# Kernel tuning notes

Measured on AMD Instinct MI355X. Metric: run time of the kernel, lower is better.

## Reference

```python
import jax, jax.numpy as jnp
import numpy as np

V = 1_000_000   # sparse_id_num
D = 64          # embedding_dim
F = 26          # sparse_feature_cnt
L = 8           # ids per feature bag (fixed-size ragged regularization)
B = 4096        # batch
IN_DIM = F * D  # 1664
HIDDENS = (1024, 1024, 512)


def setup_inputs() -> dict:
    key = jax.random.key(0)
    ks = jax.random.split(key, 4 + 4 * len(HIDDENS))
    inp = {}
    inp["x"] = jax.random.randint(ks[0], (B, F, L), 0, V, dtype=jnp.int64)
    inp["emb_table"] = jax.random.normal(ks[1], (V, D), dtype=jnp.float32) * 0.01
    ki = 2
    for i, h in enumerate(HIDDENS):
        inp[f"w1_{i}"] = jax.random.normal(ks[ki], (IN_DIM, h), dtype=jnp.float32) * 0.02
        inp[f"b1_{i}"] = jnp.zeros((h,), dtype=jnp.float32)
        inp[f"w2_{i}"] = jax.random.normal(ks[ki + 1], (h, IN_DIM), dtype=jnp.float32) * 0.02
        inp[f"b2_{i}"] = jnp.zeros((IN_DIM,), dtype=jnp.float32)
        ki += 2
    inp["lin_w"] = jax.random.normal(ks[ki], (IN_DIM, 1), dtype=jnp.float32) * 0.02
    inp["lin_b"] = jnp.zeros((1,), dtype=jnp.float32)
    return inp


def reference(x, emb_table,
              w1_0, b1_0, w2_0, b2_0,
              w1_1, b1_1, w2_1, b2_1,
              w1_2, b1_2, w2_2, b2_2,
              lin_w, lin_b):
    # Batched embedding lookup + sum-pool over bag dim + concat over features.
    # x: [B, F, L] -> gather [B, F, L, D] -> sum over L -> [B, F, D] -> [B, F*D]
    pooled = emb_table[x].sum(axis=2)              # [B, F, D]
    feat = pooled.reshape(x.shape[0], -1)          # [B, F*D]
    # Residual blocks: relu(linear2(relu(linear1(x))) + x)
    for w1, b1, w2, b2 in ((w1_0, b1_0, w2_0, b2_0),
                           (w1_1, b1_1, w2_1, b2_1),
                           (w1_2, b1_2, w2_2, b2_2)):
        h = jax.nn.relu(feat @ w1 + b1)
        feat = jax.nn.relu(h @ w2 + b2 + feat)
    return jax.nn.sigmoid(feat @ lin_w + lin_b)    # [B, 1]
```

## Files before the change

kernel.cpp:

```cpp
#include <hip/hip_runtime.h>
#include <hip/hip_bf16.h>

#define BATCH 4096
#define FEATS 26
#define BAG   8
#define EDIM  64
#define INDIM 1664

typedef short bf16x8 __attribute__((ext_vector_type(8)));
typedef float f32x4  __attribute__((ext_vector_type(4)));
typedef unsigned short u16x8 __attribute__((ext_vector_type(8)));

__device__ __forceinline__ unsigned short f2bf(float f) {
    unsigned u = __float_as_uint(f);
    unsigned r = (u + 0x7FFFu + ((u >> 16) & 1u)) >> 16;
    return (unsigned short)r;
}
__device__ __forceinline__ float bf2f(unsigned short h) {
    return __uint_as_float((unsigned)h << 16);
}
__device__ __forceinline__ void async_cp16(const void* g, void* lds_base_uniform) {
    __builtin_amdgcn_global_load_lds(
        (const __attribute__((address_space(1))) unsigned int*)g,
        (__attribute__((address_space(3))) unsigned int*)lds_base_uniform,
        16, 0, 0);
}
#define WAITCNT_VM(n) __builtin_amdgcn_s_waitcnt(0x0F70 | (n))

__global__ __launch_bounds__(256) void transpose_to_bf16(
    const float* __restrict__ in, unsigned short* __restrict__ out, int R, int C)
{
    __shared__ unsigned short tile[64][65];
    const int c0 = blockIdx.x * 64, r0 = blockIdx.y * 64;
    const int t = threadIdx.x;
    const int tc = t & 63, tr = t >> 6;
#pragma unroll
    for (int i = 0; i < 16; ++i) {
        int r = tr + i * 4;
        tile[r][tc] = f2bf(in[(long long)(r0 + r) * C + c0 + tc]);
    }
    __syncthreads();
    const int wr = t >> 3, wc = t & 7;
#pragma unroll
    for (int half = 0; half < 2; ++half) {
        int row = wr + half * 32;
        u16x8 v;
#pragma unroll
        for (int j = 0; j < 8; ++j) v[j] = tile[wc * 8 + j][row];
        *(u16x8*)(out + (long long)(c0 + row) * R + r0 + wc * 8) = v;
    }
}

__global__ __launch_bounds__(256) void embed_pool(
    const int* __restrict__ x, const float* __restrict__ emb,
    unsigned short* __restrict__ feat)
{
    int bag  = blockIdx.x * 4 + (threadIdx.x >> 6);
    int lane = threadIdx.x & 63;
    int b = bag / FEATS;
    int f = bag - b * FEATS;
    const int* xs = x + (long long)bag * BAG;
    float s = 0.f;
#pragma unroll
    for (int l = 0; l < BAG; ++l) {
        int id = xs[l];
        s += emb[(long long)id * EDIM + lane];
    }
    feat[(long long)b * INDIM + f * EDIM + lane] = f2bf(s);
}

#define NBUF 4
__global__ __launch_bounds__(512) void gemm_bf16(
    const unsigned short* __restrict__ A, const unsigned short* __restrict__ Wt,
    const float* __restrict__ bias, const unsigned short* __restrict__ res,
    unsigned short* __restrict__ out, int M, int N, int K, int do_relu)
{
    __shared__ unsigned short As[NBUF * 128 * 32];
    __shared__ unsigned short Bs[NBUF * 128 * 32];

    const int t    = threadIdx.x;
    const int bCol = blockIdx.x * 128;
    const int bRow = blockIdx.y * 128;
    const int wave = t >> 6, lane = t & 63;
    const int wm = wave & 1, wn = wave >> 1;
    const int lm = lane & 15, quad = lane >> 4;

    const int srow = lane >> 2;
    const int sq   = (lane & 3) ^ ((lane >> 3) & 3);
    const unsigned short* Ag = A  + (long long)(bRow + wave * 16 + srow) * K + sq * 8;
    const unsigned short* Bg = Wt + (long long)(bCol + wave * 16 + srow) * K + sq * 8;
    unsigned short* AsW = As + wave * 512;
    unsigned short* BsW = Bs + wave * 512;

    const int T = K / 32;
    f32x4 acc[4][2] = {};

    const int slot = (quad ^ ((lm >> 1) & 3)) * 8;

#define ISSUE(tile_)  do { int _b = (tile_) & (NBUF - 1);                         \
        async_cp16(Ag + (long long)(tile_) * 32, AsW + _b * 4096);                \
        async_cp16(Bg + (long long)(tile_) * 32, BsW + _b * 4096); } while (0)

#define COMPUTE(tile_) do { int _b = (tile_) & (NBUF - 1);                        \
        const unsigned short* _a = As + _b * 4096;                                \
        const unsigned short* _bp = Bs + _b * 4096;                               \
        bf16x8 af[4], bf[2];                                                      \
        _Pragma("unroll")                                                         \
        for (int i = 0; i < 4; ++i)                                               \
            af[i] = *(const bf16x8*)&_a[(wm * 64 + i * 16 + lm) * 32 + slot];     \
        _Pragma("unroll")                                                         \
        for (int j = 0; j < 2; ++j)                                               \
            bf[j] = *(const bf16x8*)&_bp[(wn * 32 + j * 16 + lm) * 32 + slot];    \
        _Pragma("unroll")                                                         \
        for (int i = 0; i < 4; ++i)                                               \
            _Pragma("unroll")                                                     \
            for (int j = 0; j < 2; ++j)                                           \
                acc[i][j] = __builtin_amdgcn_mfma_f32_16x16x32_bf16(              \
                    af[i], bf[j], acc[i][j], 0, 0, 0); } while (0)

    ISSUE(0);
    ISSUE(1);
    for (int tt = 0; tt < T - 2; ++tt) {
        ISSUE(tt + 2);
        WAITCNT_VM(4);
        asm volatile("" ::: "memory");
        __builtin_amdgcn_s_barrier();
        asm volatile("" ::: "memory");
        COMPUTE(tt);
    }
    WAITCNT_VM(2);
    asm volatile("" ::: "memory");
    __builtin_amdgcn_s_barrier();
    asm volatile("" ::: "memory");
    COMPUTE(T - 2);
    WAITCNT_VM(0);
    asm volatile("" ::: "memory");
    __builtin_amdgcn_s_barrier();
    asm volatile("" ::: "memory");
    COMPUTE(T - 1);

#pragma unroll
    for (int i = 0; i < 4; ++i) {
#pragma unroll
        for (int j = 0; j < 2; ++j) {
            int col = bCol + wn * 32 + j * 16 + lm;
            float bv = bias[col];
#pragma unroll
            for (int r = 0; r < 4; ++r) {
                int row = bRow + wm * 64 + i * 16 + quad * 4 + r;
                float v = acc[i][j][r] + bv;
                if (res) v += bf2f(res[(long long)row * N + col]);
                if (do_relu) v = fmaxf(v, 0.f);
                out[(long long)row * N + col] = f2bf(v);
            }
        }
    }
#undef ISSUE
#undef COMPUTE
}

__global__ __launch_bounds__(256) void final_head(
    const unsigned short* __restrict__ feat, const float* __restrict__ lin_w,
    const float* __restrict__ lin_b, float* __restrict__ out)
{
    int row  = blockIdx.x * 4 + (threadIdx.x >> 6);
    int lane = threadIdx.x & 63;
    const unsigned short* fr = feat + (long long)row * INDIM;
    float s = 0.f;
#pragma unroll
    for (int it = 0; it < INDIM / 64; ++it)
        s += bf2f(fr[it * 64 + lane]) * lin_w[it * 64 + lane];
#pragma unroll
    for (int off = 32; off; off >>= 1)
        s += __shfl_down(s, off, 64);
    if (lane == 0)
        out[row] = 1.f / (1.f + __expf(-(s + lin_b[0])));
}

extern "C" void kernel_launch(void* const* d_in, const int* in_sizes, int n_in,
                              void* d_out, int out_size, void* d_ws, size_t ws_size,
                              hipStream_t stream) {
    const int*   x    = (const int*)  d_in[0];
    const float* emb  = (const float*)d_in[1];
    const float* w1_0 = (const float*)d_in[2];
    const float* b1_0 = (const float*)d_in[3];
    const float* w2_0 = (const float*)d_in[4];
    const float* b2_0 = (const float*)d_in[5];
    const float* w1_1 = (const float*)d_in[6];
    const float* b1_1 = (const float*)d_in[7];
    const float* w2_1 = (const float*)d_in[8];
    const float* b2_1 = (const float*)d_in[9];
    const float* w1_2 = (const float*)d_in[10];
    const float* b1_2 = (const float*)d_in[11];
    const float* w2_2 = (const float*)d_in[12];
    const float* b2_2 = (const float*)d_in[13];
    const float* linw = (const float*)d_in[14];
    const float* linb = (const float*)d_in[15];
    float* out = (float*)d_out;

    unsigned short* feat = (unsigned short*)d_ws;
    unsigned short* h    = feat + (long long)BATCH * INDIM;
    unsigned short* p    = h + (long long)BATCH * 1024;
    unsigned short* w1_0t = p; p += 1024 * INDIM;
    unsigned short* w2_0t = p; p += INDIM * 1024;
    unsigned short* w1_1t = p; p += 1024 * INDIM;
    unsigned short* w2_1t = p; p += INDIM * 1024;
    unsigned short* w1_2t = p; p += 512 * INDIM;
    unsigned short* w2_2t = p; p += INDIM * 512;

    transpose_to_bf16<<<dim3(1024/64, INDIM/64), 256, 0, stream>>>(w1_0, w1_0t, INDIM, 1024);
    transpose_to_bf16<<<dim3(INDIM/64, 1024/64), 256, 0, stream>>>(w2_0, w2_0t, 1024, INDIM);
    transpose_to_bf16<<<dim3(1024/64, INDIM/64), 256, 0, stream>>>(w1_1, w1_1t, INDIM, 1024);
    transpose_to_bf16<<<dim3(INDIM/64, 1024/64), 256, 0, stream>>>(w2_1, w2_1t, 1024, INDIM);
    transpose_to_bf16<<<dim3(512/64,  INDIM/64), 256, 0, stream>>>(w1_2, w1_2t, INDIM, 512);
    transpose_to_bf16<<<dim3(INDIM/64, 512/64),  256, 0, stream>>>(w2_2, w2_2t, 512, INDIM);

    embed_pool<<<BATCH * FEATS / 4, 256, 0, stream>>>(x, emb, feat);

    gemm_bf16<<<dim3(1024/128, BATCH/128), 512, 0, stream>>>(
        feat, w1_0t, b1_0, nullptr, h, BATCH, 1024, INDIM, 1);
    gemm_bf16<<<dim3(INDIM/128, BATCH/128), 512, 0, stream>>>(
        h, w2_0t, b2_0, feat, feat, BATCH, INDIM, 1024, 1);
    gemm_bf16<<<dim3(1024/128, BATCH/128), 512, 0, stream>>>(
        feat, w1_1t, b1_1, nullptr, h, BATCH, 1024, INDIM, 1);
    gemm_bf16<<<dim3(INDIM/128, BATCH/128), 512, 0, stream>>>(
        h, w2_1t, b2_1, feat, feat, BATCH, INDIM, 1024, 1);
    gemm_bf16<<<dim3(512/128, BATCH/128), 512, 0, stream>>>(
        feat, w1_2t, b1_2, nullptr, h, BATCH, 512, INDIM, 1);
    gemm_bf16<<<dim3(INDIM/128, BATCH/128), 512, 0, stream>>>(
        h, w2_2t, b2_2, feat, feat, BATCH, INDIM, 512, 1);

    final_head<<<BATCH / 4, 256, 0, stream>>>(feat, linw, linb, out);
}
```

Measured before the change: 568.6 us.

## Merge weight transposes into one launch and window embedding gathers by address

The six weight-transpose launches become one 3D-grid kernel that picks its matrix from blockIdx.z, with out-of-range blocks exiting early. The embedding pooling now has each wave handle four bags and loads all 32 ids up front. It then walks 31 address windows of 2M floats each, issuing only the gathers whose row falls in the current window. This is meant to keep concurrent gathers across the GPU in a narrow part of the 256MB table for better cache and TLB locality, and to save launch overhead. The cost is 31 passes of predicate checks per wave, and the loop stays correct only because every offset lies below 31·2^21.

After: 763.0 us. +34.2%, slower.

```diff
diff --git a/kernel.cpp b/kernel.cpp
--- a/kernel.cpp
+++ b/kernel.cpp
@@ -1,5 +1,4 @@
 #include <hip/hip_runtime.h>
-#include <hip/hip_bf16.h>
 
 #define BATCH 4096
 #define FEATS 26
@@ -27,11 +26,27 @@
 }
 #define WAITCNT_VM(n) __builtin_amdgcn_s_waitcnt(0x0F70 | (n))
 
-__global__ __launch_bounds__(256) void transpose_to_bf16(
-    const float* __restrict__ in, unsigned short* __restrict__ out, int R, int C)
-{
+__global__ __launch_bounds__(256) void transpose_all(
+    const float* __restrict__ w10, unsigned short* __restrict__ o10,
+    const float* __restrict__ w20, unsigned short* __restrict__ o20,
+    const float* __restrict__ w11, unsigned short* __restrict__ o11,
+    const float* __restrict__ w21, unsigned short* __restrict__ o21,
+    const float* __restrict__ w12, unsigned short* __restrict__ o12,
+    const float* __restrict__ w22, unsigned short* __restrict__ o22)
+{
+    const float* in; unsigned short* out; int R, C;
+    switch (blockIdx.z) {
+        case 0:  in = w10; out = o10; R = INDIM; C = 1024;  break;
+        case 1:  in = w20; out = o20; R = 1024;  C = INDIM; break;
+        case 2:  in = w11; out = o11; R = INDIM; C = 1024;  break;
+        case 3:  in = w21; out = o21; R = 1024;  C = INDIM; break;
+        case 4:  in = w12; out = o12; R = INDIM; C = 512;   break;
+        default: in = w22; out = o22; R = 512;   C = INDIM; break;
+    }
+    const int c0 = blockIdx.x * 64, r0 = blockIdx.y * 64;
+    if (c0 >= C || r0 >= R) return;
+
     __shared__ unsigned short tile[64][65];
-    const int c0 = blockIdx.x * 64, r0 = blockIdx.y * 64;
     const int t = threadIdx.x;
     const int tc = t & 63, tr = t >> 6;
 #pragma unroll
@@ -51,22 +66,39 @@
     }
 }
 
+#define BPW 4
+#define NWIN 31
 __global__ __launch_bounds__(256) void embed_pool(
     const int* __restrict__ x, const float* __restrict__ emb,
     unsigned short* __restrict__ feat)
 {
-    int bag  = blockIdx.x * 4 + (threadIdx.x >> 6);
-    int lane = threadIdx.x & 63;
-    int b = bag / FEATS;
-    int f = bag - b * FEATS;
-    const int* xs = x + (long long)bag * BAG;
-    float s = 0.f;
-#pragma unroll
-    for (int l = 0; l < BAG; ++l) {
-        int id = xs[l];
-        s += emb[(long long)id * EDIM + lane];
-    }
-    feat[(long long)b * INDIM + f * EDIM + lane] = f2bf(s);
+    const int wave = threadIdx.x >> 6, lane = threadIdx.x & 63;
+    const int bag0 = (blockIdx.x * 4 + wave) * BPW;
+    const float* embl = emb + lane;
+
+    unsigned off[BPW][BAG];
+#pragma unroll
+    for (int g = 0; g < BPW; ++g)
+#pragma unroll
+        for (int l = 0; l < BAG; ++l)
+            off[g][l] = (unsigned)x[(bag0 + g) * BAG + l] * (unsigned)EDIM;
+
+    float s[BPW] = {};
+#pragma unroll 1
+    for (unsigned w = 0; w < NWIN; ++w) {
+#pragma unroll
+        for (int g = 0; g < BPW; ++g)
+#pragma unroll
+            for (int l = 0; l < BAG; ++l)
+                if ((off[g][l] >> 21) == w)
+                    s[g] += embl[off[g][l]];
+    }
+#pragma unroll
+    for (int g = 0; g < BPW; ++g) {
+        int bag = bag0 + g;
+        int b = bag / FEATS, f = bag - b * FEATS;
+        feat[(long long)b * INDIM + f * EDIM + lane] = f2bf(s[g]);
+    }
 }
 
 #define NBUF 4
@@ -94,7 +126,6 @@
 
     const int T = K / 32;
     f32x4 acc[4][2] = {};
-
     const int slot = (quad ^ ((lm >> 1) & 3)) * 8;
 
 #define ISSUE(tile_)  do { int _b = (tile_) & (NBUF - 1);                         \
@@ -208,14 +239,10 @@
     unsigned short* w1_2t = p; p += 512 * INDIM;
     unsigned short* w2_2t = p; p += INDIM * 512;
 
-    transpose_to_bf16<<<dim3(1024/64, INDIM/64), 256, 0, stream>>>(w1_0, w1_0t, INDIM, 1024);
-    transpose_to_bf16<<<dim3(INDIM/64, 1024/64), 256, 0, stream>>>(w2_0, w2_0t, 1024, INDIM);
-    transpose_to_bf16<<<dim3(1024/64, INDIM/64), 256, 0, stream>>>(w1_1, w1_1t, INDIM, 1024);
-    transpose_to_bf16<<<dim3(INDIM/64, 1024/64), 256, 0, stream>>>(w2_1, w2_1t, 1024, INDIM);
-    transpose_to_bf16<<<dim3(512/64,  INDIM/64), 256, 0, stream>>>(w1_2, w1_2t, INDIM, 512);
-    transpose_to_bf16<<<dim3(INDIM/64, 512/64),  256, 0, stream>>>(w2_2, w2_2t, 512, INDIM);
-
-    embed_pool<<<BATCH * FEATS / 4, 256, 0, stream>>>(x, emb, feat);
+    transpose_all<<<dim3(26, 26, 6), 256, 0, stream>>>(
+        w1_0, w1_0t, w2_0, w2_0t, w1_1, w1_1t, w2_1, w2_1t, w1_2, w1_2t, w2_2, w2_2t);
+
+    embed_pool<<<BATCH * FEATS / (4 * BPW), 256, 0, stream>>>(x, emb, feat);
 
     gemm_bf16<<<dim3(1024/128, BATCH/128), 512, 0, stream>>>(
         feat, w1_0t, b1_0, nullptr, h, BATCH, 1024, INDIM, 1);
```

## Use 4-wave GEMM blocks with double buffering and batch weight transposes

Applied to the files above, without the earlier changes.

The GEMM moves from 8 waves per block with a 4-deep async LDS pipeline to 4 waves per block with launch bounds allowing 3 blocks per CU and a 2-stage buffer. Each wave now computes a 64x64 (or 64x32) sub-tile, and the kernel is templated on BN so the N=512 layer uses 64-wide tiles to get more blocks. The six weight-transpose launches are merged into one 3D-grid launch to cut launch overhead. The shallower pipeline and the full waitcnt plus barrier on every K step may expose more memory latency, relying on extra occupancy to hide it.

New measurement: 603.0 us. 6.1% more time.

```diff
diff --git a/kernel.cpp b/kernel.cpp
--- a/kernel.cpp
+++ b/kernel.cpp
@@ -1,5 +1,4 @@
 #include <hip/hip_runtime.h>
-#include <hip/hip_bf16.h>
 
 #define BATCH 4096
 #define FEATS 26
@@ -27,11 +26,27 @@
 }
 #define WAITCNT_VM(n) __builtin_amdgcn_s_waitcnt(0x0F70 | (n))
 
-__global__ __launch_bounds__(256) void transpose_to_bf16(
-    const float* __restrict__ in, unsigned short* __restrict__ out, int R, int C)
-{
+__global__ __launch_bounds__(256) void transpose_all(
+    const float* __restrict__ w10, unsigned short* __restrict__ o10,
+    const float* __restrict__ w20, unsigned short* __restrict__ o20,
+    const float* __restrict__ w11, unsigned short* __restrict__ o11,
+    const float* __restrict__ w21, unsigned short* __restrict__ o21,
+    const float* __restrict__ w12, unsigned short* __restrict__ o12,
+    const float* __restrict__ w22, unsigned short* __restrict__ o22)
+{
+    const float* in; unsigned short* out; int R, C;
+    switch (blockIdx.z) {
+        case 0:  in = w10; out = o10; R = INDIM; C = 1024;  break;
+        case 1:  in = w20; out = o20; R = 1024;  C = INDIM; break;
+        case 2:  in = w11; out = o11; R = INDIM; C = 1024;  break;
+        case 3:  in = w21; out = o21; R = 1024;  C = INDIM; break;
+        case 4:  in = w12; out = o12; R = INDIM; C = 512;   break;
+        default: in = w22; out = o22; R = 512;   C = INDIM; break;
+    }
+    const int c0 = blockIdx.x * 64, r0 = blockIdx.y * 64;
+    if (c0 >= C || r0 >= R) return;
+
     __shared__ unsigned short tile[64][65];
-    const int c0 = blockIdx.x * 64, r0 = blockIdx.y * 64;
     const int t = threadIdx.x;
     const int tc = t & 63, tr = t >> 6;
 #pragma unroll
@@ -69,17 +84,20 @@
     feat[(long long)b * INDIM + f * EDIM + lane] = f2bf(s);
 }
 
-#define NBUF 4
-__global__ __launch_bounds__(512) void gemm_bf16(
+#define NBUF 2
+template<int BN>
+__global__ __launch_bounds__(256, 3) void gemm_bf16(
     const unsigned short* __restrict__ A, const unsigned short* __restrict__ Wt,
     const float* __restrict__ bias, const unsigned short* __restrict__ res,
     unsigned short* __restrict__ out, int M, int N, int K, int do_relu)
 {
+    constexpr int JN = BN / 32;
+
     __shared__ unsigned short As[NBUF * 128 * 32];
-    __shared__ unsigned short Bs[NBUF * 128 * 32];
+    __shared__ unsigned short Bs[NBUF * BN * 32];
 
     const int t    = threadIdx.x;
-    const int bCol = blockIdx.x * 128;
+    const int bCol = blockIdx.x * BN;
     const int bRow = blockIdx.y * 128;
     const int wave = t >> 6, lane = t & 63;
     const int wm = wave & 1, wn = wave >> 1;
@@ -87,63 +105,62 @@
 
     const int srow = lane >> 2;
     const int sq   = (lane & 3) ^ ((lane >> 3) & 3);
-    const unsigned short* Ag = A  + (long long)(bRow + wave * 16 + srow) * K + sq * 8;
-    const unsigned short* Bg = Wt + (long long)(bCol + wave * 16 + srow) * K + sq * 8;
-    unsigned short* AsW = As + wave * 512;
-    unsigned short* BsW = Bs + wave * 512;
+    const int slot = (quad ^ ((lm >> 1) & 3)) * 8;
+
+    const unsigned short* Ag  = A + (long long)(bRow + wave * 32 + srow) * K + sq * 8;
+    const unsigned short* Ag2 = Ag + 16 * (long long)K;
+    const unsigned short* Bg  = Wt + (long long)(bCol + (BN == 128 ? wave * 32 : wave * 16) + srow) * K + sq * 8;
+    const unsigned short* Bg2 = Bg + 16 * (long long)K;
+    unsigned short* AsW = As + wave * 1024;
+    unsigned short* BsW = Bs + wave * (BN == 128 ? 1024 : 512);
 
     const int T = K / 32;
-    f32x4 acc[4][2] = {};
-
-    const int slot = (quad ^ ((lm >> 1) & 3)) * 8;
-
-#define ISSUE(tile_)  do { int _b = (tile_) & (NBUF - 1);                         \
-        async_cp16(Ag + (long long)(tile_) * 32, AsW + _b * 4096);                \
-        async_cp16(Bg + (long long)(tile_) * 32, BsW + _b * 4096); } while (0)
-
-#define COMPUTE(tile_) do { int _b = (tile_) & (NBUF - 1);                        \
-        const unsigned short* _a = As + _b * 4096;                                \
-        const unsigned short* _bp = Bs + _b * 4096;                               \
-        bf16x8 af[4], bf[2];                                                      \
+    f32x4 acc[4][JN] = {};
+
+#define ISSUE(t_)  do { int _b = (t_) & 1;                                        \
+        async_cp16(Ag  + (t_) * 32, AsW + _b * 4096);                             \
+        async_cp16(Ag2 + (t_) * 32, AsW + _b * 4096 + 512);                       \
+        async_cp16(Bg  + (t_) * 32, BsW + _b * (BN * 32));                        \
+        if constexpr (BN == 128)                                                  \
+            async_cp16(Bg2 + (t_) * 32, BsW + _b * (BN * 32) + 512);              \
+    } while (0)
+
+#define COMPUTE(t_) do { int _b = (t_) & 1;                                       \
+        const unsigned short* _a  = As + _b * 4096;                               \
+        const unsigned short* _bp = Bs + _b * (BN * 32);                          \
+        bf16x8 af[4], bfr[JN];                                                    \
         _Pragma("unroll")                                                         \
         for (int i = 0; i < 4; ++i)                                               \
             af[i] = *(const bf16x8*)&_a[(wm * 64 + i * 16 + lm) * 32 + slot];     \
         _Pragma("unroll")                                                         \
-        for (int j = 0; j < 2; ++j)                                               \
-            bf[j] = *(const bf16x8*)&_bp[(wn * 32 + j * 16 + lm) * 32 + slot];    \
+        for (int j = 0; j < JN; ++j)                                              \
+            bfr[j] = *(const bf16x8*)&_bp[(wn * (BN / 2) + j * 16 + lm) * 32 + slot]; \
         _Pragma("unroll")                                                         \
         for (int i = 0; i < 4; ++i)                                               \
             _Pragma("unroll")                                                     \
-            for (int j = 0; j < 2; ++j)                                           \
+            for (int j = 0; j < JN; ++j)                                          \
                 acc[i][j] = __builtin_amdgcn_mfma_f32_16x16x32_bf16(              \
-                    af[i], bf[j], acc[i][j], 0, 0, 0); } while (0)
+                    af[i], bfr[j], acc[i][j], 0, 0, 0); } while (0)
 
     ISSUE(0);
-    ISSUE(1);
-    for (int tt = 0; tt < T - 2; ++tt) {
-        ISSUE(tt + 2);
-        WAITCNT_VM(4);
-        asm volatile("" ::: "memory");
-        __builtin_amdgcn_s_barrier();
-        asm volatile("" ::: "memory");
-        COMPUTE(tt);
-    }
-    WAITCNT_VM(2);
-    asm volatile("" ::: "memory");
-    __builtin_amdgcn_s_barrier();
-    asm volatile("" ::: "memory");
-    COMPUTE(T - 2);
     WAITCNT_VM(0);
     asm volatile("" ::: "memory");
     __builtin_amdgcn_s_barrier();
     asm volatile("" ::: "memory");
-    COMPUTE(T - 1);
+    for (int tt = 0; tt < T; ++tt) {
+        if (tt + 1 < T) ISSUE(tt + 1);
+        COMPUTE(tt);
+        WAITCNT_VM(0);
+        asm volatile("" ::: "memory");
+        __builtin_amdgcn_s_barrier();
+        asm volatile("" ::: "memory");
+    }
 
 #pragma unroll
     for (int i = 0; i < 4; ++i) {
 #pragma unroll
-        for (int j = 0; j < 2; ++j) {
-            int col = bCol + wn * 32 + j * 16 + lm;
+        for (int j = 0; j < JN; ++j) {
+            int col = bCol + wn * (BN / 2) + j * 16 + lm;
             float bv = bias[col];
 #pragma unroll
             for (int r = 0; r < 4; ++r) {
@@ -208,26 +225,22 @@
     unsigned short* w1_2t = p; p += 512 * INDIM;
     unsigned short* w2_2t = p; p += INDIM * 512;
 
-    transpose_to_bf16<<<dim3(1024/64, INDIM/64), 256, 0, stream>>>(w1_0, w1_0t, INDIM, 1024);
-    transpose_to_bf16<<<dim3(INDIM/64, 1024/64), 256, 0, stream>>>(w2_0, w2_0t, 1024, INDIM);
-    transpose_to_bf16<<<dim3(1024/64, INDIM/64), 256, 0, stream>>>(w1_1, w1_1t, INDIM, 1024);
-    transpose_to_bf16<<<dim3(INDIM/64, 1024/64), 256, 0, stream>>>(w2_1, w2_1t, 1024, INDIM);
-    transpose_to_bf16<<<dim3(512/64,  INDIM/64), 256, 0, stream>>>(w1_2, w1_2t, INDIM, 512);
-    transpose_to_bf16<<<dim3(INDIM/64, 512/64),  256, 0, stream>>>(w2_2, w2_2t, 512, INDIM);
+    transpose_all<<<dim3(26, 26, 6), 256, 0, stream>>>(
+        w1_0, w1_0t, w2_0, w2_0t, w1_1, w1_1t, w2_1, w2_1t, w1_2, w1_2t, w2_2, w2_2t);
 
     embed_pool<<<BATCH * FEATS / 4, 256, 0, stream>>>(x, emb, feat);
 
-    gemm_bf16<<<dim3(1024/128, BATCH/128), 512, 0, stream>>>(
+    gemm_bf16<128><<<dim3(1024/128, BATCH/128), 256, 0, stream>>>(
         feat, w1_0t, b1_0, nullptr, h, BATCH, 1024, INDIM, 1);
-    gemm_bf16<<<dim3(INDIM/128, BATCH/128), 512, 0, stream>>>(
+    gemm_bf16<128><<<dim3(INDIM/128, BATCH/128), 256, 0, stream>>>(
         h, w2_0t, b2_0, feat, feat, BATCH, INDIM, 1024, 1);
-    gemm_bf16<<<dim3(1024/128, BATCH/128), 512, 0, stream>>>(
+    gemm_bf16<128><<<dim3(1024/128, BATCH/128), 256, 0, stream>>>(
         feat, w1_1t, b1_1, nullptr, h, BATCH, 1024, INDIM, 1);
-    gemm_bf16<<<dim3(INDIM/128, BATCH/128), 512, 0, stream>>>(
+    gemm_bf16<128><<<dim3(INDIM/128, BATCH/128), 256, 0, stream>>>(
         h, w2_1t, b2_1, feat, feat, BATCH, INDIM, 1024, 1);
-    gemm_bf16<<<dim3(512/128, BATCH/128), 512, 0, stream>>>(
+    gemm_bf16<64><<<dim3(512/64, BATCH/128), 256, 0, stream>>>(
         feat, w1_2t, b1_2, nullptr, h, BATCH, 512, INDIM, 1);
-    gemm_bf16<<<dim3(INDIM/128, BATCH/128), 512, 0, stream>>>(
+    gemm_bf16<128><<<dim3(INDIM/128, BATCH/128), 256, 0, stream>>>(
         h, w2_2t, b2_2, feat, feat, BATCH, INDIM, 512, 1);
 
     final_head<<<BATCH / 4, 256, 0, stream>>>(feat, linw, linb, out);
```
